# Kernel tuning notes

Hardware: AMD Instinct MI355X
Metric: run time of the kernel (lower is better)

Reference implementation:

```python
import jax, jax.numpy as jnp
import numpy as np

B, OBS, ACT, NT, E = 4096, 512, 64, 10, 16
DREP, DH, DK = 1024, 1024, 512  # rep dim, expert hidden, key/value dim


def setup_inputs() -> dict:
    key = jax.random.key(0)
    ks = jax.random.split(key, 24)
    s = 0.02
    state_core = jax.random.normal(ks[0], (B, OBS), jnp.float32)
    task_ids = jax.random.randint(ks[1], (B,), 0, NT)
    onehot = jax.nn.one_hot(task_ids, NT, dtype=jnp.float32)
    state = jnp.concatenate([state_core, onehot], axis=-1)  # [B, OBS+NT]
    act = jax.random.normal(ks[2], (B, ACT), jnp.float32)
    return {
        "state": state,
        "act": act,
        "rep_W0": s * jax.random.normal(ks[3], (OBS + ACT, DREP), jnp.float32),
        "rep_b0": jnp.zeros((DREP,), jnp.float32),
        "rep_W1": s * jax.random.normal(ks[4], (DREP, DREP), jnp.float32),
        "rep_b1": jnp.zeros((DREP,), jnp.float32),
        "emb": 0.5 * jnp.ones((NT, DK), jnp.float32),
        "Wk0": s * jax.random.normal(ks[5], (E, DREP, DH), jnp.float32),
        "bk0": jnp.zeros((E, DH), jnp.float32),
        "Wk1": s * jax.random.normal(ks[6], (E, DH, DK), jnp.float32),
        "bk1": jnp.zeros((E, DK), jnp.float32),
        "Wv0": s * jax.random.normal(ks[7], (E, DREP, DH), jnp.float32),
        "bv0": jnp.zeros((E, DH), jnp.float32),
        "Wv1": s * jax.random.normal(ks[8], (E, DH, DK), jnp.float32),
        "bv1": jnp.zeros((E, DK), jnp.float32),
        "Wt0": s * jax.random.normal(ks[9], (DK, 512), jnp.float32),
        "bt0": jnp.zeros((512,), jnp.float32),
        "Wt1": s * jax.random.normal(ks[10], (512, 256), jnp.float32),
        "bt1": jnp.zeros((256,), jnp.float32),
        "Wt2": s * jax.random.normal(ks[11], (256, 1), jnp.float32),
        "bt2": jnp.zeros((1,), jnp.float32),
    }


def reference(state, act, rep_W0, rep_b0, rep_W1, rep_b1, emb,
              Wk0, bk0, Wk1, bk1, Wv0, bv0, Wv1, bv1,
              Wt0, bt0, Wt1, bt1, Wt2, bt2):
    num_tasks = emb.shape[0]
    task = jnp.argmax(state[:, -num_tasks:], axis=-1)  # one-hot -> index (== torch.nonzero)
    s = state[:, :-num_tasks]
    # representation: mlp([obs+act, 1024, 1024]) -> relu then identity
    x = jnp.concatenate([s, act], axis=-1)
    rep = jax.nn.relu(x @ rep_W0 + rep_b0) @ rep_W1 + rep_b1  # [B, DREP]
    query = jnp.tanh(emb[task])  # [B, DK]
    # all experts batched (original loops in Python over E tiny MLPs)
    hk = jax.nn.relu(jnp.einsum('bd,edh->ebh', rep, Wk0) + bk0[:, None, :])
    keys = jnp.einsum('ebh,ehk->ebk', hk, Wk1) + bk1[:, None, :]   # [E,B,DK]
    hv = jax.nn.relu(jnp.einsum('bd,edh->ebh', rep, Wv0) + bv0[:, None, :])
    vals = jnp.einsum('ebh,ehk->ebk', hv, Wv1) + bv1[:, None, :]   # [E,B,DK]
    logits = jnp.einsum('bk,ebk->be', query, keys)                 # [B,E]
    attn = jax.nn.softmax(logits, axis=1)
    tower_in = jnp.einsum('be,ebk->bk', attn, vals)                # [B,DK]
    h = jax.nn.relu(tower_in @ Wt0 + bt0)
    h = jax.nn.relu(h @ Wt1 + bt1)
    q = jnp.squeeze(h @ Wt2 + bt2, -1)                             # [B]
    expert_loss = -jnp.mean(
        jnp.sum(jnp.clip(jnp.log(attn + 1e-10), -6.0, 0.0), axis=-1) * 0.3)
    return q, expert_loss
```

## Files before the change

### kernel.cpp

```cpp
#include <hip/hip_runtime.h>
#include <cstdint>
#include <cstddef>

#define NB   4096
#define OBS  512
#define NACT 64
#define NT   10
#define NE   16
#define DREP 1024
#define DH   1024
#define DK   512
#define SLD  (OBS + NT)
#define XK   (OBS + NACT)

typedef short s8v __attribute__((ext_vector_type(8)));
typedef float f4v __attribute__((ext_vector_type(4)));

__device__ __forceinline__ unsigned short f2bf(float f) {
  union { float f; unsigned int u; } v; v.f = f;
  unsigned int u = v.u;
  unsigned int r = (u + 0x7FFFu + ((u >> 16) & 1u)) >> 16;
  return (unsigned short)r;
}
__device__ __forceinline__ float bf2f(unsigned short h) {
  union { unsigned int u; float f; } v; v.u = ((unsigned int)h) << 16;
  return v.f;
}

__device__ __forceinline__ void gload_lds16(const unsigned short* gp, const unsigned short* lp) {
  __builtin_amdgcn_global_load_lds(
      (const __attribute__((address_space(1))) void*)(uintptr_t)gp,
      (__attribute__((address_space(3))) void*)(unsigned int)(uintptr_t)lp,
      16, 0, 0);
}

template <int BM, int BN, int MODE, int RELU, int LDA, int LDB, int KK>
__global__ void __launch_bounds__(256)
gemm_k(const unsigned short* __restrict__ A,
       const unsigned short* __restrict__ Bt,
       const float* __restrict__ bias,
       unsigned short* __restrict__ outB, int ldo,
       const float* __restrict__ qk1, const int* __restrict__ task,
       float* __restrict__ logits, int eBase,
       const float* __restrict__ attn, float* __restrict__ cio)
{
  constexpr int FM = BM / 32;
  constexpr int FN = BN / 32;
  constexpr int CA = BM / 64;
  constexpr int CB = BN / 64;
  constexpr int NTILES = KK / 32;
  static_assert(NTILES >= 3, "pipeline depth");
  constexpr int LPS = CA + CB;
  static_assert(LPS < 16, "vmcnt immediate fits in low bits");
  constexpr int WAIT_STAGE = 0xF70 | LPS;
  constexpr int WAIT_ALL   = 0xF70;

  __shared__ __align__(16) unsigned short As[3][BM * 32];
  __shared__ __align__(16) unsigned short Bs[3][BN * 32];

  const int tid  = threadIdx.x;
  const int wave = tid >> 6;
  const int lane = tid & 63;
  const int wm = wave >> 1, wn = wave & 1;

  const int rowBase = blockIdx.x * BM;
  const int colBase = blockIdx.y * BN;

  if (MODE == 3 || MODE == 4) {
    A   += (size_t)blockIdx.z * KK;
    Bt  += (size_t)blockIdx.z * KK;
    cio += (size_t)blockIdx.z * NB * DK;
  }

  f4v acc[FM][FN];
#pragma unroll
  for (int m = 0; m < FM; ++m)
#pragma unroll
    for (int n = 0; n < FN; ++n) acc[m][n] = f4v{0.f, 0.f, 0.f, 0.f};

  const int sRow = lane >> 2;
  const int sSw  = ((lane & 3) ^ ((sRow >> 1) & 3)) * 8;

  const unsigned short* ag[CA];
  const unsigned short* bg[CB];
#pragma unroll
  for (int j = 0; j < CA; ++j)
    ag[j] = A + (size_t)(rowBase + (wave * CA + j) * 16 + sRow) * LDA + sSw;
#pragma unroll
  for (int j = 0; j < CB; ++j)
    bg[j] = Bt + (size_t)(colBase + (wave * CB + j) * 16 + sRow) * LDB + sSw;

  const int fr   = lane & 15;
  const int koSw = ((lane >> 4) ^ ((fr >> 1) & 3)) * 8;
  const int aOff = (wm * (BM / 2) + fr) * 32 + koSw;
  const int bOff = (wn * (BN / 2) + fr) * 32 + koSw;

  auto stage = [&](int buf) {
#pragma unroll
    for (int j = 0; j < CA; ++j) { gload_lds16(ag[j], &As[buf][(wave * CA + j) * 512]); ag[j] += 32; }
#pragma unroll
    for (int j = 0; j < CB; ++j) { gload_lds16(bg[j], &Bs[buf][(wave * CB + j) * 512]); bg[j] += 32; }
  };

  auto compute = [&](int buf) {
    s8v av[FM], bv[FN];
#pragma unroll
    for (int m = 0; m < FM; ++m)
      av[m] = *reinterpret_cast<const s8v*>(&As[buf][aOff + m * 512]);
#pragma unroll
    for (int n = 0; n < FN; ++n)
      bv[n] = *reinterpret_cast<const s8v*>(&Bs[buf][bOff + n * 512]);
#pragma unroll
    for (int m = 0; m < FM; ++m)
#pragma unroll
      for (int n = 0; n < FN; ++n)
        acc[m][n] = __builtin_amdgcn_mfma_f32_16x16x32_bf16(av[m], bv[n], acc[m][n], 0, 0, 0);
  };

  stage(0);
  stage(1);

  for (int t = 0; t < NTILES; t += 3) {
    if (t + 1 < NTILES) __builtin_amdgcn_s_waitcnt(WAIT_STAGE);
    else                __builtin_amdgcn_s_waitcnt(WAIT_ALL);
    __builtin_amdgcn_s_barrier();
    if (t + 2 < NTILES) stage(2);
    compute(0);
    if (t + 1 < NTILES) {
      if (t + 2 < NTILES) __builtin_amdgcn_s_waitcnt(WAIT_STAGE);
      else                __builtin_amdgcn_s_waitcnt(WAIT_ALL);
      __builtin_amdgcn_s_barrier();
      if (t + 3 < NTILES) stage(0);
      compute(1);
    }
    if (t + 2 < NTILES) {
      if (t + 3 < NTILES) __builtin_amdgcn_s_waitcnt(WAIT_STAGE);
      else                __builtin_amdgcn_s_waitcnt(WAIT_ALL);
      __builtin_amdgcn_s_barrier();
      if (t + 4 < NTILES) stage(1);
      compute(2);
    }
  }

  const int cr = (lane >> 4) * 4;
  const int cc = lane & 15;

  int gcn[FN];
  float bcol[FN];
#pragma unroll
  for (int n = 0; n < FN; ++n) {
    gcn[n] = colBase + wn * (BN / 2) + n * 16 + cc;
    bcol[n] = (MODE >= 3) ? 0.f : bias[gcn[n]];
  }

  if (MODE == 0) {
#pragma unroll
    for (int m = 0; m < FM; ++m)
#pragma unroll
      for (int r = 0; r < 4; ++r) {
        int gr = rowBase + wm * (BM / 2) + m * 16 + cr + r;
#pragma unroll
        for (int n = 0; n < FN; ++n) {
          float v = acc[m][n][r] + bcol[n];
          if (RELU) v = fmaxf(v, 0.f);
          outB[(size_t)gr * ldo + gcn[n]] = f2bf(v);
        }
      }
  }

  if (MODE == 3 || MODE == 4) {
#pragma unroll
    for (int m = 0; m < FM; ++m)
#pragma unroll
      for (int r = 0; r < 4; ++r) {
        int gr = rowBase + wm * (BM / 2) + m * 16 + cr + r;
#pragma unroll
        for (int n = 0; n < FN; ++n) {
          float v = acc[m][n][r];
          if (MODE == 4) v += cio[(size_t)gr * DK + gcn[n]];
          cio[(size_t)gr * DK + gcn[n]] = v;
        }
      }
  }
}

template <int MODE, int LDA, int LDB, int KK>
__global__ void __launch_bounds__(512)
gemm256_k(const unsigned short* __restrict__ A,
          const unsigned short* __restrict__ Bt,
          const float* __restrict__ bias,
          unsigned short* __restrict__ outB, int ldo,
          const float* __restrict__ qk1, const int* __restrict__ task,
          float* __restrict__ logits, int eBase,
          const float* __restrict__ attn)
{
  constexpr int NTK = KK / 64;
  static_assert(NTK >= 4 && (NTK & 1) == 0, "pipeline depth");

  __shared__ __align__(16) unsigned short As[2][16384];
  __shared__ __align__(16) unsigned short Bs[2][16384];

  const int tid  = threadIdx.x;
  const int wave = tid >> 6;
  const int lane = tid & 63;

  const int rowBase = blockIdx.x * 256;
  const int colBase = blockIdx.y * 256;

  int eg = 0;
  if (MODE == 1) {
    eg = blockIdx.z;
    Bt   += (size_t)eg * ((size_t)DREP * DH);
    bias += eg * DH;
    qk1  += (size_t)eg * (NT * DH);
  }
  if (MODE == 2) {
    eg = eBase + blockIdx.z;
    Bt   += (size_t)eg * ((size_t)DREP * DH);
    bias += eg * DH;
    outB += (size_t)blockIdx.z * DH;
  }

  f4v acc[2][2][2][4];
#pragma unroll
  for (int i0 = 0; i0 < 2; ++i0)
#pragma unroll
    for (int i1 = 0; i1 < 2; ++i1)
#pragma unroll
      for (int i2 = 0; i2 < 2; ++i2)
#pragma unroll
        for (int i3 = 0; i3 < 4; ++i3)
          acc[i0][i1][i2][i3] = f4v{0.f, 0.f, 0.f, 0.f};

  const int l3 = lane >> 3, l7 = lane & 7, l4 = lane >> 4;
  size_t srcA[2], srcB[2];
#pragma unroll
  for (int j = 0; j < 2; ++j) {
    const int r  = j * 64 + wave * 8 + l3;
    const int ks = (l7 ^ l3) * 8;
    srcA[j] = (size_t)(rowBase + r) * LDA + ks;
    srcB[j] = (size_t)(colBase + r) * LDB + ks;
  }

  auto stageA = [&](int buf, int half, int t) {
#pragma unroll
    for (int j = 0; j < 2; ++j)
      gload_lds16(A + srcA[j] + (size_t)half * (128 * LDA) + t * 64,
                  &As[buf][half * 8192 + j * 4096 + wave * 512]);
  };
  auto stageB = [&](int buf, int half, int t) {
#pragma unroll
    for (int j = 0; j < 2; ++j)
      gload_lds16(Bt + srcB[j] + (size_t)half * (128 * LDB) + t * 64,
                  &Bs[buf][half * 8192 + j * 4096 + wave * 512]);
  };

  const int cOff0 = (l4 ^ l7) * 8;
  const int cOff1 = ((4 + l4) ^ l7) * 8;
  const int aRowOff = ((wave & 3) * 32 + (lane & 15)) * 64;
  const int bColOff = ((wave >> 2) * 64 + (lane & 15)) * 64;

  s8v av[2][2], bv[4][2];
  auto readA = [&](int buf, int qm) {
#pragma unroll
    for (int f = 0; f < 2; ++f) {
      const unsigned short* p = &As[buf][qm * 8192 + aRowOff + f * 1024];
      av[f][0] = *reinterpret_cast<const s8v*>(p + cOff0);
      av[f][1] = *reinterpret_cast<const s8v*>(p + cOff1);
    }
  };
  auto readB = [&](int buf, int qn) {
#pragma unroll
    for (int fc = 0; fc < 4; ++fc) {
      const unsigned short* p = &Bs[buf][qn * 8192 + bColOff + fc * 1024];
      bv[fc][0] = *reinterpret_cast<const s8v*>(p + cOff0);
      bv[fc][1] = *reinterpret_cast<const s8v*>(p + cOff1);
    }
  };

#define MFMA_BLK(QM, QN)                                                      \
  do {                                                                        \
    __builtin_amdgcn_s_setprio(1);                                            \
    _Pragma("unroll") for (int ks_ = 0; ks_ < 2; ++ks_)                       \
      _Pragma("unroll") for (int f_ = 0; f_ < 2; ++f_)                        \
        _Pragma("unroll") for (int fc_ = 0; fc_ < 4; ++fc_)                   \
          acc[QM][QN][f_][fc_] = __builtin_amdgcn_mfma_f32_16x16x32_bf16(     \
              av[f_][ks_], bv[fc_][ks_], acc[QM][QN][f_][fc_], 0, 0, 0);      \
    __builtin_amdgcn_s_setprio(0);                                            \
  } while (0)

  stageA(0, 0, 0); stageB(0, 0, 0); stageA(0, 1, 0); stageB(0, 1, 0);
  stageB(1, 0, 1); stageA(1, 1, 1);
  __builtin_amdgcn_s_waitcnt(0xF74);
  __builtin_amdgcn_s_barrier();

  for (int t = 0; t < NTK; ++t) {
    const int buf = t & 1;
    readA(buf, 0); readB(buf, 0);
    if (t + 1 < NTK) stageA(buf ^ 1, 0, t + 1);
    __builtin_amdgcn_s_barrier();
    MFMA_BLK(0, 0);
    __builtin_amdgcn_s_barrier();
    readA(buf, 1);
    if (t + 1 < NTK) stageB(buf ^ 1, 1, t + 1);
    __builtin_amdgcn_s_barrier();
    MFMA_BLK(1, 0);
    __builtin_amdgcn_s_barrier();
    readB(buf, 1);
    if (t + 2 < NTK) stageB(buf, 0, t + 2);
    __builtin_amdgcn_s_barrier();
    MFMA_BLK(1, 1);
    __builtin_amdgcn_s_barrier();
    readA(buf, 0);
    if (t + 2 < NTK) stageA(buf, 1, t + 2);
    if (t + 2 < NTK)      __builtin_amdgcn_s_waitcnt(0xF74);
    else if (t + 1 < NTK) __builtin_amdgcn_s_waitcnt(0xF70);
    __builtin_amdgcn_s_barrier();
    MFMA_BLK(0, 1);
    __builtin_amdgcn_s_barrier();
  }
#undef MFMA_BLK

  const int cr = l4 * 4;
  const int cc = lane & 15;

  int gcn[2][4];
  float bcol[2][4];
#pragma unroll
  for (int qn = 0; qn < 2; ++qn)
#pragma unroll
    for (int fc = 0; fc < 4; ++fc) {
      gcn[qn][fc]  = colBase + qn * 128 + (wave >> 2) * 64 + fc * 16 + cc;
      bcol[qn][fc] = bias[gcn[qn][fc]];
    }

  if (MODE == 1) {
#pragma unroll
    for (int qm = 0; qm < 2; ++qm)
#pragma unroll
      for (int f = 0; f < 2; ++f)
#pragma unroll
        for (int r = 0; r < 4; ++r) {
          const int gr = rowBase + qm * 128 + (wave & 3) * 32 + f * 16 + cr + r;
          const float* qrow = qk1 + (size_t)task[gr] * DH;
          float s = 0.f;
#pragma unroll
          for (int qn = 0; qn < 2; ++qn)
#pragma unroll
            for (int fc = 0; fc < 4; ++fc) {
              float v = fmaxf(acc[qm][qn][f][fc][r] + bcol[qn][fc], 0.f);
              s += v * qrow[gcn[qn][fc]];
            }
#pragma unroll
          for (int off = 1; off < 16; off <<= 1) s += __shfl_xor(s, off, 64);
          if (cc == 0) atomicAdd(&logits[gr * NE + eg], s);
        }
  }

  if (MODE == 2) {
#pragma unroll
    for (int qm = 0; qm < 2; ++qm)
#pragma unroll
      for (int f = 0; f < 2; ++f)
#pragma unroll
        for (int r = 0; r < 4; ++r) {
          const int gr = rowBase + qm * 128 + (wave & 3) * 32 + f * 16 + cr + r;
          const float aw = attn[gr * NE + eg];
#pragma unroll
          for (int qn = 0; qn < 2; ++qn)
#pragma unroll
            for (int fc = 0; fc < 4; ++fc) {
              float v = fmaxf(acc[qm][qn][f][fc][r] + bcol[qn][fc], 0.f) * aw;
              outB[(size_t)gr * ldo + gcn[qn][fc]] = f2bf(v);
            }
        }
  }
}

__global__ void task_k(const float* __restrict__ state, int* __restrict__ task) {
  int b = blockIdx.x * blockDim.x + threadIdx.x;
  if (b >= NB) return;
  const float* p = state + (size_t)b * SLD + OBS;
  float best = p[0]; int bi = 0;
  for (int j = 1; j < NT; ++j) { float v = p[j]; if (v > best) { best = v; bi = j; } }
  task[b] = bi;
}

__global__ void buildx_k(const float* __restrict__ state, const float* __restrict__ act,
                         unsigned short* __restrict__ x) {
  int idx = blockIdx.x * blockDim.x + threadIdx.x;
  if (idx >= NB * XK) return;
  int b = idx / XK, j = idx - b * XK;
  float v = (j < OBS) ? state[(size_t)b * SLD + j] : act[(size_t)b * NACT + (j - OBS)];
  x[idx] = f2bf(v);
}

__global__ void prep_emb_k(const float* __restrict__ emb, const float* __restrict__ bk1,
                           float* __restrict__ Qt, float* __restrict__ qb) {
  int t = blockIdx.x;
  __shared__ float qsh[DK];
  for (int k = threadIdx.x; k < DK; k += 256) {
    float v = tanhf(emb[t * DK + k]);
    Qt[t * DK + k] = v;
    qsh[k] = v;
  }
  __syncthreads();
  int wave = threadIdx.x >> 6, lane = threadIdx.x & 63;
  for (int e = wave; e < NE; e += 4) {
    float s = 0.f;
    for (int k = lane; k < DK; k += 64) s += qsh[k] * bk1[e * DK + k];
    for (int off = 1; off < 64; off <<= 1) s += __shfl_xor(s, off, 64);
    if (lane == 0) qb[e * NT + t] = s;
  }
}

__global__ void qk1_k(const float* __restrict__ Wk1, const float* __restrict__ Qt,
                      float* __restrict__ qk1) {
  int w = (blockIdx.x * blockDim.x + threadIdx.x) >> 6;
  int lane = threadIdx.x & 63;
  if (w >= NE * DH) return;
  int e = w >> 10, h = w & (DH - 1);
  const float* wrow = Wk1 + ((size_t)e * DH + h) * DK + lane * 8;
  float wv[8];
#pragma unroll
  for (int j = 0; j < 8; ++j) wv[j] = wrow[j];
#pragma unroll
  for (int t = 0; t < NT; ++t) {
    const float* qrow = Qt + t * DK + lane * 8;
    float s = 0.f;
#pragma unroll
    for (int j = 0; j < 8; ++j) s += wv[j] * qrow[j];
#pragma unroll
    for (int off = 1; off < 64; off <<= 1) s += __shfl_xor(s, off, 64);
    if (lane == 0) qk1[((size_t)e * NT + t) * DH + h] = s;
  }
}

__global__ void __launch_bounds__(256)
convT_k(const float* __restrict__ src, unsigned short* __restrict__ dst,
        int N, long sBS, long dBS, int dLd) {
  __shared__ float tile[64][65];
  int e = blockIdx.z;
  int n0 = blockIdx.x * 64, k0 = blockIdx.y * 64;
  src += (size_t)e * sBS + (size_t)k0 * N + n0;
  dst += (size_t)e * dBS + (size_t)n0 * dLd + k0;
  int t = threadIdx.x;
  int c4 = t & 15, kr = t >> 4;
#pragma unroll
  for (int i = 0; i < 4; ++i) {
    float4 v = *(const float4*)(src + (size_t)(kr + i * 16) * N + c4 * 4);
    tile[kr + i * 16][c4 * 4 + 0] = v.x;
    tile[kr + i * 16][c4 * 4 + 1] = v.y;
    tile[kr + i * 16][c4 * 4 + 2] = v.z;
    tile[kr + i * 16][c4 * 4 + 3] = v.w;
  }
  __syncthreads();
  int sub = t & 7, nl = t >> 3;
#pragma unroll
  for (int pass = 0; pass < 2; ++pass) {
    int n = nl + pass * 32;
    unsigned short v8[8];
#pragma unroll
    for (int j = 0; j < 8; ++j) v8[j] = f2bf(tile[sub * 8 + j][n]);
    *reinterpret_cast<s8v*>(dst + (size_t)n * dLd + sub * 8) =
        *reinterpret_cast<const s8v*>(v8);
  }
}

__global__ void softmax_k(const float* __restrict__ logits, const float* __restrict__ qb,
                          const int* __restrict__ task, float* __restrict__ attn,
                          float* __restrict__ lossOut) {
  int b = blockIdx.x * blockDim.x + threadIdx.x;
  int t = task[b];
  float l[NE];
  float mx = -1e30f;
#pragma unroll
  for (int e = 0; e < NE; ++e) { l[e] = logits[b * NE + e] + qb[e * NT + t]; mx = fmaxf(mx, l[e]); }
  float s = 0.f;
#pragma unroll
  for (int e = 0; e < NE; ++e) { l[e] = expf(l[e] - mx); s += l[e]; }
  float inv = 1.f / s;
  float loss = 0.f;
#pragma unroll
  for (int e = 0; e < NE; ++e) {
    float a = l[e] * inv;
    attn[b * NE + e] = a;
    float lg = logf(a + 1e-10f);
    loss += fminf(fmaxf(lg, -6.f), 0.f);
  }
  for (int off = 1; off < 64; off <<= 1) loss += __shfl_xor(loss, off, 64);
  if ((threadIdx.x & 63) == 0) atomicAdd(lossOut, loss * (-0.3f / NB));
}

__global__ void towerbias_k(const float* __restrict__ attn, const float* __restrict__ bv1,
                            float* __restrict__ towerin) {
  int idx = blockIdx.x * blockDim.x + threadIdx.x;
  if (idx >= NB * DK) return;
  int b = idx >> 9, k = idx & (DK - 1);
  float s = 0.f;
#pragma unroll
  for (int e = 0; e < NE; ++e) s += attn[b * NE + e] * bv1[e * DK + k];
  towerin[idx] = s;
}

__global__ void cvt_ti_k(const float* __restrict__ twin, const float* __restrict__ P,
                         unsigned short* __restrict__ ti) {
  int idx = (blockIdx.x * blockDim.x + threadIdx.x) * 8;
  if (idx >= NB * DK) return;
  float v[8];
#pragma unroll
  for (int j = 0; j < 8; ++j) v[j] = twin[idx + j];
#pragma unroll
  for (int c = 0; c < 4; ++c) {
    const float* p = P + (size_t)c * NB * DK + idx;
#pragma unroll
    for (int j = 0; j < 8; ++j) v[j] += p[j];
  }
  unsigned short v8[8];
#pragma unroll
  for (int j = 0; j < 8; ++j) v8[j] = f2bf(v[j]);
  *reinterpret_cast<s8v*>(ti + idx) = *reinterpret_cast<const s8v*>(v8);
}

__global__ void qfinal_k(const unsigned short* __restrict__ h2, const float* __restrict__ Wt2,
                         const float* __restrict__ bt2, float* __restrict__ out) {
  int w = (blockIdx.x * blockDim.x + threadIdx.x) >> 6;
  int lane = threadIdx.x & 63;
  if (w >= NB) return;
  float s = 0.f;
#pragma unroll
  for (int j = 0; j < 4; ++j) {
    int k = lane * 4 + j;
    s += bf2f(h2[(size_t)w * 256 + k]) * Wt2[k];
  }
  for (int off = 1; off < 64; off <<= 1) s += __shfl_xor(s, off, 64);
  if (lane == 0) out[w] = s + bt2[0];
}

extern "C" void kernel_launch(void* const* d_in, const int* in_sizes, int n_in,
                              void* d_out, int out_size, void* d_ws, size_t ws_size,
                              hipStream_t stream) {
  const float* state  = (const float*)d_in[0];
  const float* act    = (const float*)d_in[1];
  const float* rep_W0 = (const float*)d_in[2];
  const float* rep_b0 = (const float*)d_in[3];
  const float* rep_W1 = (const float*)d_in[4];
  const float* rep_b1 = (const float*)d_in[5];
  const float* emb    = (const float*)d_in[6];
  const float* Wk0    = (const float*)d_in[7];
  const float* bk0    = (const float*)d_in[8];
  const float* Wk1    = (const float*)d_in[9];
  const float* bk1    = (const float*)d_in[10];
  const float* Wv0    = (const float*)d_in[11];
  const float* bv0    = (const float*)d_in[12];
  const float* Wv1    = (const float*)d_in[13];
  const float* bv1    = (const float*)d_in[14];
  const float* Wt0    = (const float*)d_in[15];
  const float* bt0    = (const float*)d_in[16];
  const float* Wt1    = (const float*)d_in[17];
  const float* bt1    = (const float*)d_in[18];
  const float* Wt2    = (const float*)d_in[19];
  const float* bt2    = (const float*)d_in[20];
  float* out = (float*)d_out;

  char* wsb = (char*)d_ws;
  size_t off = 0;
  auto alloc = [&](size_t bytes) -> void* {
    void* p = wsb + off;
    off += (bytes + 255) & ~(size_t)255;
    return p;
  };
  unsigned short* Ap    = (unsigned short*)alloc((size_t)NB * 8192 * 2);
  unsigned short* Wk0t  = (unsigned short*)alloc((size_t)NE * DREP * DH * 2);
  unsigned short* Wv0t  = (unsigned short*)alloc((size_t)NE * DREP * DH * 2);
  unsigned short* Wv1t  = (unsigned short*)alloc((size_t)DK * (NE * DH) * 2);
  float*          P     = (float*)alloc((size_t)4 * NB * DK * 4);
  unsigned short* h0    = (unsigned short*)alloc((size_t)NB * DREP * 2);
  unsigned short* rep   = (unsigned short*)alloc((size_t)NB * DREP * 2);
  float*          twin  = (float*)alloc((size_t)NB * DK * 4);
  unsigned short* xbuf  = (unsigned short*)alloc((size_t)NB * XK * 2);
  unsigned short* ti    = (unsigned short*)alloc((size_t)NB * DK * 2);
  unsigned short* h1    = (unsigned short*)alloc((size_t)NB * 512 * 2);
  unsigned short* h2    = (unsigned short*)alloc((size_t)NB * 256 * 2);
  unsigned short* rW1t  = (unsigned short*)alloc((size_t)DREP * DREP * 2);
  unsigned short* rW0t  = (unsigned short*)alloc((size_t)DREP * XK * 2);
  float*          qk1   = (float*)alloc((size_t)NE * NT * DH * 4);
  unsigned short* Wt0t  = (unsigned short*)alloc((size_t)512 * 512 * 2);
  unsigned short* Wt1t  = (unsigned short*)alloc((size_t)256 * 512 * 2);
  float*          logits= (float*)alloc((size_t)NB * NE * 4);
  float*          attn  = (float*)alloc((size_t)NB * NE * 4);
  float*          Qt    = (float*)alloc((size_t)NT * DK * 4);
  int*            task  = (int*)alloc((size_t)NB * 4);
  float*          qb    = (float*)alloc((size_t)NE * NT * 4);

  hipMemsetAsync(logits, 0, (size_t)NB * NE * 4, stream);
  hipMemsetAsync(out + NB, 0, sizeof(float), stream);

  task_k<<<NB / 256, 256, 0, stream>>>(state, task);
  buildx_k<<<(NB * XK + 255) / 256, 256, 0, stream>>>(state, act, xbuf);
  prep_emb_k<<<NT, 256, 0, stream>>>(emb, bk1, Qt, qb);
  qk1_k<<<NE * DH / 4, 256, 0, stream>>>(Wk1, Qt, qk1);

  convT_k<<<dim3(DREP / 64, XK / 64, 1), 256, 0, stream>>>(rep_W0, rW0t, DREP, 0, 0, XK);
  convT_k<<<dim3(DREP / 64, DREP / 64, 1), 256, 0, stream>>>(rep_W1, rW1t, DREP, 0, 0, DREP);
  convT_k<<<dim3(DH / 64, DREP / 64, NE), 256, 0, stream>>>(Wk0, Wk0t, DH, (long)DREP * DH, (long)DREP * DH, DREP);
  convT_k<<<dim3(DH / 64, DREP / 64, NE), 256, 0, stream>>>(Wv0, Wv0t, DH, (long)DREP * DH, (long)DREP * DH, DREP);
  convT_k<<<dim3(DK / 64, DH / 64, NE), 256, 0, stream>>>(Wv1, Wv1t, DK, (long)DH * DK, 1024L, NE * DH);
  convT_k<<<dim3(512 / 64, 512 / 64, 1), 256, 0, stream>>>(Wt0, Wt0t, 512, 0, 0, 512);
  convT_k<<<dim3(256 / 64, 512 / 64, 1), 256, 0, stream>>>(Wt1, Wt1t, 256, 0, 0, 512);

  gemm_k<128, 128, 0, 1, XK, XK, XK><<<dim3(NB / 128, DREP / 128, 1), 256, 0, stream>>>(
      xbuf, rW0t, rep_b0, h0, DREP, nullptr, nullptr, nullptr, 0, nullptr, nullptr);
  gemm_k<128, 128, 0, 0, DREP, DREP, DREP><<<dim3(NB / 128, DREP / 128, 1), 256, 0, stream>>>(
      h0, rW1t, rep_b1, rep, DREP, nullptr, nullptr, nullptr, 0, nullptr, nullptr);

  gemm256_k<1, DREP, DREP, DREP><<<dim3(NB / 256, DH / 256, NE), 512, 0, stream>>>(
      rep, Wk0t, bk0, nullptr, 0, qk1, task, logits, 0, nullptr);

  softmax_k<<<NB / 256, 256, 0, stream>>>(logits, qb, task, attn, out + NB);
  towerbias_k<<<NB * DK / 256, 256, 0, stream>>>(attn, bv1, twin);

  for (int g = 0; g < 2; ++g) {
    gemm256_k<2, DREP, DREP, DREP><<<dim3(NB / 256, DH / 256, 8), 512, 0, stream>>>(
        rep, Wv0t, bv0, Ap, 8192, nullptr, nullptr, nullptr, g * 8, attn);
    if (g == 0)
      gemm_k<128, 128, 3, 0, 8192, NE * DH, 2048><<<dim3(NB / 128, DK / 128, 4), 256, 0, stream>>>(
          Ap, Wv1t, nullptr, nullptr, 0, nullptr, nullptr, nullptr, 0, nullptr, P);
    else
      gemm_k<128, 128, 4, 0, 8192, NE * DH, 2048><<<dim3(NB / 128, DK / 128, 4), 256, 0, stream>>>(
          Ap, Wv1t + (size_t)8192, nullptr, nullptr, 0, nullptr, nullptr, nullptr, 0, nullptr, P);
  }
  cvt_ti_k<<<(NB * DK / 8 + 255) / 256, 256, 0, stream>>>(twin, P, ti);

  gemm_k<64, 64, 0, 1, DK, DK, DK><<<dim3(NB / 64, 512 / 64, 1), 256, 0, stream>>>(
      ti, Wt0t, bt0, h1, 512, nullptr, nullptr, nullptr, 0, nullptr, nullptr);
  gemm_k<64, 64, 0, 1, 512, 512, 512><<<dim3(NB / 64, 256 / 64, 1), 256, 0, stream>>>(
      h1, Wt1t, bt1, h2, 256, nullptr, nullptr, nullptr, 0, nullptr, nullptr);
  qfinal_k<<<NB / 4, 256, 0, stream>>>(h2, Wt2, bt2, out);
}
```

Before: 746.1 us.

## Remap workgroups across XCDs and restructure GEMM pipeline with fewer barriers

Workgroup IDs are remapped so that consecutive tiles are spread round-robin across the 8 XCDs, with the expert and column indices derived from the remapped flat ID. This is meant to improve L2 locality of shared B and A tiles. The main loop keeps two A fragment register sets so the A half is not re-read, drops four of eight barriers per tile, reorders the stage issue, and unrolls by two with constant buffer indices. Global load pointers are now advanced incrementally instead of being recomputed. The reduced barriers carry a risk of LDS read/write races if the reordered stage timing is wrong.

After: 824.7 us. 1.11x slower.

```diff
diff --git a/kernel.cpp b/kernel.cpp
--- a/kernel.cpp
+++ b/kernel.cpp
@@ -203,22 +203,31 @@
   const int tid  = threadIdx.x;
   const int wave = tid >> 6;
   const int lane = tid & 63;
-
-  const int rowBase = blockIdx.x * 256;
-  const int colBase = blockIdx.y * 256;
+  const int l3 = lane >> 3, l7 = lane & 7, l4 = lane >> 4;
+
+  const int gx = gridDim.x, gy = gridDim.y;
+  int flat = blockIdx.x + gx * (blockIdx.y + gy * blockIdx.z);
+  const int nwg = gx * gy * gridDim.z;
+  flat = (flat & 7) * (nwg >> 3) + (flat >> 3);
+  const int bx = flat % gx; flat /= gx;
+  const int by = flat % gy;
+  const int bz = flat / gy;
+
+  const int rowBase = bx * 256;
+  const int colBase = by * 256;
 
   int eg = 0;
   if (MODE == 1) {
-    eg = blockIdx.z;
+    eg = bz;
     Bt   += (size_t)eg * ((size_t)DREP * DH);
     bias += eg * DH;
     qk1  += (size_t)eg * (NT * DH);
   }
   if (MODE == 2) {
-    eg = eBase + blockIdx.z;
+    eg = eBase + bz;
     Bt   += (size_t)eg * ((size_t)DREP * DH);
     bias += eg * DH;
-    outB += (size_t)blockIdx.z * DH;
+    outB += (size_t)bz * DH;
   }
 
   f4v acc[2][2][2][4];
@@ -232,27 +241,31 @@
         for (int i3 = 0; i3 < 4; ++i3)
           acc[i0][i1][i2][i3] = f4v{0.f, 0.f, 0.f, 0.f};
 
-  const int l3 = lane >> 3, l7 = lane & 7, l4 = lane >> 4;
-  size_t srcA[2], srcB[2];
-#pragma unroll
-  for (int j = 0; j < 2; ++j) {
-    const int r  = j * 64 + wave * 8 + l3;
-    const int ks = (l7 ^ l3) * 8;
-    srcA[j] = (size_t)(rowBase + r) * LDA + ks;
-    srcB[j] = (size_t)(colBase + r) * LDB + ks;
-  }
-
-  auto stageA = [&](int buf, int half, int t) {
-#pragma unroll
-    for (int j = 0; j < 2; ++j)
-      gload_lds16(A + srcA[j] + (size_t)half * (128 * LDA) + t * 64,
-                  &As[buf][half * 8192 + j * 4096 + wave * 512]);
-  };
-  auto stageB = [&](int buf, int half, int t) {
-#pragma unroll
-    for (int j = 0; j < 2; ++j)
-      gload_lds16(Bt + srcB[j] + (size_t)half * (128 * LDB) + t * 64,
-                  &Bs[buf][half * 8192 + j * 4096 + wave * 512]);
+  const unsigned short* pA[2][2];
+  const unsigned short* pB[2][2];
+#pragma unroll
+  for (int h = 0; h < 2; ++h)
+#pragma unroll
+    for (int j = 0; j < 2; ++j) {
+      const int r  = h * 128 + j * 64 + wave * 8 + l3;
+      const int ks = (l7 ^ l3) * 8;
+      pA[h][j] = A  + (size_t)(rowBase + r) * LDA + ks;
+      pB[h][j] = Bt + (size_t)(colBase + r) * LDB + ks;
+    }
+
+  auto stageA = [&](int buf, int h) {
+#pragma unroll
+    for (int j = 0; j < 2; ++j) {
+      gload_lds16(pA[h][j], &As[buf][h * 8192 + j * 4096 + wave * 512]);
+      pA[h][j] += 64;
+    }
+  };
+  auto stageB = [&](int buf, int h) {
+#pragma unroll
+    for (int j = 0; j < 2; ++j) {
+      gload_lds16(pB[h][j], &Bs[buf][h * 8192 + j * 4096 + wave * 512]);
+      pB[h][j] += 64;
+    }
   };
 
   const int cOff0 = (l4 ^ l7) * 8;
@@ -260,11 +273,11 @@
   const int aRowOff = ((wave & 3) * 32 + (lane & 15)) * 64;
   const int bColOff = ((wave >> 2) * 64 + (lane & 15)) * 64;
 
-  s8v av[2][2], bv[4][2];
-  auto readA = [&](int buf, int qm) {
+  s8v avA[2][2], avB[2][2], bv[4][2];
+  auto readAh = [&](int buf, int h, s8v (&av)[2][2]) {
 #pragma unroll
     for (int f = 0; f < 2; ++f) {
-      const unsigned short* p = &As[buf][qm * 8192 + aRowOff + f * 1024];
+      const unsigned short* p = &As[buf][h * 8192 + aRowOff + f * 1024];
       av[f][0] = *reinterpret_cast<const s8v*>(p + cOff0);
       av[f][1] = *reinterpret_cast<const s8v*>(p + cOff1);
     }
@@ -278,46 +291,46 @@
     }
   };
 
-#define MFMA_BLK(QM, QN)                                                      \
+#define MFMA_BLK(QM, QN, AV)                                                  \
   do {                                                                        \
     __builtin_amdgcn_s_setprio(1);                                            \
     _Pragma("unroll") for (int ks_ = 0; ks_ < 2; ++ks_)                       \
       _Pragma("unroll") for (int f_ = 0; f_ < 2; ++f_)                        \
         _Pragma("unroll") for (int fc_ = 0; fc_ < 4; ++fc_)                   \
           acc[QM][QN][f_][fc_] = __builtin_amdgcn_mfma_f32_16x16x32_bf16(     \
-              av[f_][ks_], bv[fc_][ks_], acc[QM][QN][f_][fc_], 0, 0, 0);      \
+              AV[f_][ks_], bv[fc_][ks_], acc[QM][QN][f_][fc_], 0, 0, 0);      \
     __builtin_amdgcn_s_setprio(0);                                            \
   } while (0)
 
-  stageA(0, 0, 0); stageB(0, 0, 0); stageA(0, 1, 0); stageB(0, 1, 0);
-  stageB(1, 0, 1); stageA(1, 1, 1);
-  __builtin_amdgcn_s_waitcnt(0xF74);
-  __builtin_amdgcn_s_barrier();
-
-  for (int t = 0; t < NTK; ++t) {
-    const int buf = t & 1;
-    readA(buf, 0); readB(buf, 0);
-    if (t + 1 < NTK) stageA(buf ^ 1, 0, t + 1);
+  auto tile_body = [&](int t, int buf) __attribute__((always_inline)) {
+    readAh(buf, 0, avA);
+    readB(buf, 0);
+    if (t + 1 < NTK) stageB(buf ^ 1, 1);
     __builtin_amdgcn_s_barrier();
-    MFMA_BLK(0, 0);
+    MFMA_BLK(0, 0, avA);
+    readAh(buf, 1, avB);
+    if (t + 1 < NTK) stageA(buf ^ 1, 0);
     __builtin_amdgcn_s_barrier();
-    readA(buf, 1);
-    if (t + 1 < NTK) stageB(buf ^ 1, 1, t + 1);
+    MFMA_BLK(1, 0, avB);
+    readB(buf, 1);
+    if (t + 2 < NTK) stageB(buf, 0);
     __builtin_amdgcn_s_barrier();
-    MFMA_BLK(1, 0);
-    __builtin_amdgcn_s_barrier();
-    readB(buf, 1);
-    if (t + 2 < NTK) stageB(buf, 0, t + 2);
-    __builtin_amdgcn_s_barrier();
-    MFMA_BLK(1, 1);
-    __builtin_amdgcn_s_barrier();
-    readA(buf, 0);
-    if (t + 2 < NTK) stageA(buf, 1, t + 2);
+    MFMA_BLK(1, 1, avB);
+    if (t + 2 < NTK) stageA(buf, 1);
     if (t + 2 < NTK)      __builtin_amdgcn_s_waitcnt(0xF74);
     else if (t + 1 < NTK) __builtin_amdgcn_s_waitcnt(0xF70);
     __builtin_amdgcn_s_barrier();
-    MFMA_BLK(0, 1);
-    __builtin_amdgcn_s_barrier();
+    MFMA_BLK(0, 1, avA);
+  };
+
+  stageA(0, 0); stageB(0, 0); stageA(0, 1); stageB(0, 1);
+  stageB(1, 0); stageA(1, 1);
+  __builtin_amdgcn_s_waitcnt(0xF74);
+  __builtin_amdgcn_s_barrier();
+
+  for (int t = 0; t < NTK; t += 2) {
+    tile_body(t, 0);
+    tile_body(t + 1, 1);
   }
 #undef MFMA_BLK
 
```
